# Kernel optimization log

Hardware: AMD Instinct MI355X
Metric: run time of the kernel (lower is better)

Reference implementation:

```python
import jax, jax.numpy as jnp
import numpy as np

BATCH, K, N, D = 8192, 8, 1024, 256
BETA = 0.25


def setup_inputs() -> dict:
    key = jax.random.key(0)
    kx, ke = jax.random.split(key)
    x = jax.random.normal(kx, (BATCH, K, D), dtype=jnp.float32)
    entries = jax.random.normal(ke, (K, N, D), dtype=jnp.float32)
    return {"x": x, "entries": entries}


def reference(x, entries):
    # x: [b, k, d]; entries: [k, n, d]
    xt = jnp.transpose(x, (1, 0, 2))  # [k, b, d]
    # squared euclidean distances (argmin is identical to cdist argmin)
    d2 = (
        jnp.sum(xt * xt, axis=-1)[:, :, None]
        + jnp.sum(entries * entries, axis=-1)[:, None, :]
        - 2.0 * jnp.einsum("kbd,knd->kbn", xt, entries)
    )  # [k, b, n]
    idx = jnp.argmin(d2, axis=-1)  # [k, b]
    quantized = jnp.take_along_axis(entries, idx[:, :, None], axis=1)  # [k, b, d]
    quantized = jnp.transpose(quantized, (1, 0, 2))  # [b, k, d]
    # straight-through estimator
    x_q = x + jax.lax.stop_gradient(quantized - x)
    dictionary_loss = jnp.mean(
        jnp.sum((jax.lax.stop_gradient(x) - quantized) ** 2, axis=-1)
    )
    commitment_loss = BETA * jnp.mean(
        jnp.sum((x - jax.lax.stop_gradient(quantized)) ** 2, axis=-1)
    )
    return x_q, jnp.transpose(idx, (1, 0)), dictionary_loss, commitment_loss
```

## Files before the change

### kernel.cpp

```cpp
#include <hip/hip_runtime.h>
#include <cstdint>
#include <cstddef>

#define BATCH 8192
#define KC 8
#define NC 1024
#define DC 256
#define TAU 0.10f

typedef __attribute__((ext_vector_type(8))) _Float16 half8;
typedef __attribute__((ext_vector_type(4))) _Float16 half4;
typedef __attribute__((ext_vector_type(4))) float floatx4;

__device__ __forceinline__ void async_load16(const void* g, void* l) {
    __builtin_amdgcn_global_load_lds((const __attribute__((address_space(1))) uint32_t*)g,
                                     (__attribute__((address_space(3))) uint32_t*)l, 16, 0, 0);
}

__device__ __forceinline__ int lidx(int r, int c) {
    return (r >> 3) * 1024 + (r & 7) * 128 + ((c ^ (r & 7)) * 16);
}
__device__ __forceinline__ half8 ldsr(const char* base, int r, int c) {
    return *(const half8*)(base + lidx(r, c));
}

__global__ __launch_bounds__(256) void prep_e_kernel(const float* __restrict__ entries,
                                                     _Float16* __restrict__ Ecat,
                                                     float* __restrict__ eef) {
    int wave = threadIdx.x >> 6, lane = threadIdx.x & 63;
    int row = blockIdx.x * 4 + wave;
    float4 v = ((const float4*)(entries + (size_t)row * DC))[lane];
    half4 h;
    h.x = (_Float16)v.x; h.y = (_Float16)v.y; h.z = (_Float16)v.z; h.w = (_Float16)v.w;
    *(half4*)(Ecat + (size_t)row * 256 + lane * 4) = h;
    double s = (double)v.x * v.x + (double)v.y * v.y + (double)v.z * v.z + (double)v.w * v.w;
    #pragma unroll
    for (int off = 32; off > 0; off >>= 1) s += __shfl_down(s, off, 64);
    if (lane == 0) eef[row] = (float)s;
}

__global__ __launch_bounds__(256, 2) void vq_gemm(const float* __restrict__ x,
                                                  const float* __restrict__ entries,
                                                  const _Float16* __restrict__ Ecat,
                                                  const float* __restrict__ eef,
                                                  float* __restrict__ out_idx,
                                                  float* __restrict__ out_q,
                                                  double* __restrict__ partial,
                                                  int* __restrict__ flag_list,
                                                  int* __restrict__ flag_cnt) {
    __shared__ alignas(16) char Bst[2][32768];
    __shared__ float eef_lds[NC];
    __shared__ float tv1[128];
    __shared__ float tv2[128];
    __shared__ int   ti1[128];
    __shared__ int   idx_lds[128];
    __shared__ double red[256];

    const int t = threadIdx.x;
    const int k  = blockIdx.x & 7;
    const int b0 = (blockIdx.x >> 3) * 128;
    const int w = t >> 6, lane = t & 63;
    const int quad = lane >> 4, col = lane & 15;
    const int rl = lane >> 3;
    const int cs = (lane & 7) ^ rl;

    { float4 v = ((const float4*)(eef + (size_t)k * NC))[t]; *(float4*)(eef_lds + t * 4) = v; }
    if (t < 128) { tv1[t] = 1e30f; tv2[t] = 1e30f; ti1[t] = 0; }

    half8 Ah[2][8];
    #pragma unroll
    for (int mi = 0; mi < 2; ++mi) {
        const float* xrow = x + ((size_t)(b0 + w * 32 + mi * 16 + col) * KC + k) * DC + quad * 8;
        #pragma unroll
        for (int ks = 0; ks < 8; ++ks) {
            float4 u0 = *(const float4*)(xrow + ks * 32);
            float4 u1 = *(const float4*)(xrow + ks * 32 + 4);
            float f[8] = {u0.x, u0.y, u0.z, u0.w, u1.x, u1.y, u1.z, u1.w};
            half8 h;
            #pragma unroll
            for (int j = 0; j < 8; ++j) h[j] = (_Float16)f[j];
            Ah[mi][ks] = h;
        }
    }

    const char* EcatK = (const char*)(Ecat + (size_t)k * NC * 256);

    #define ISSUE_B(nt_, h_)                                                             \
        {                                                                                \
            char* bb_ = Bst[h_];                                                         \
            _Pragma("unroll")                                                            \
            for (int j = 0; j < 8; ++j) {                                                \
                int li_ = w * 8 + j; int sub_ = li_ >> 4, grp_ = li_ & 15;               \
                const char* src_ = EcatK + (size_t)((nt_) * 128 + grp_ * 8 + rl) * 512   \
                                 + ((h_) * 128 + sub_ * 64) * 2 + cs * 16;               \
                async_load16(src_, bb_ + sub_ * 16384 + grp_ * 1024 + lane * 16);        \
            }                                                                            \
        }

    #define STAGE(h_, DOISS_, nti_)                                                      \
        {                                                                                \
            asm volatile("s_waitcnt vmcnt(0)" ::: "memory");                             \
            __builtin_amdgcn_s_barrier();                                                \
            __builtin_amdgcn_sched_barrier(0);                                           \
            if (DOISS_) { ISSUE_B((nti_), (h_) ^ 1); }                                   \
            const char* Bs_ = Bst[h_];                                                   \
            __builtin_amdgcn_s_setprio(1);                                               \
            _Pragma("unroll")                                                            \
            for (int sub = 0; sub < 2; ++sub) {                                          \
                _Pragma("unroll")                                                        \
                for (int kk = 0; kk < 2; ++kk) {                                         \
                    const int cb = kk * 4 + quad;                                        \
                    _Pragma("unroll")                                                    \
                    for (int ni = 0; ni < 8; ++ni) {                                     \
                        half8 bh = ldsr(Bs_ + sub * 16384, ni * 16 + col, cb);           \
                        acc[0][ni] = __builtin_amdgcn_mfma_f32_16x16x32_f16(             \
                            Ah[0][(h_) * 4 + sub * 2 + kk], bh, acc[0][ni], 0, 0, 0);    \
                        acc[1][ni] = __builtin_amdgcn_mfma_f32_16x16x32_f16(             \
                            Ah[1][(h_) * 4 + sub * 2 + kk], bh, acc[1][ni], 0, 0, 0);    \
                    }                                                                    \
                }                                                                        \
            }                                                                            \
            __builtin_amdgcn_s_setprio(0);                                               \
        }

    ISSUE_B(0, 0);

    for (int nt = 0; nt < 8; ++nt) {
        const int n0 = nt * 128;
        floatx4 acc[2][8] = {};
        STAGE(0, 1, nt)
        STAGE(1, (nt < 7), nt + 1)
        float ev[8];
        #pragma unroll
        for (int ni = 0; ni < 8; ++ni) ev[ni] = eef_lds[n0 + ni * 16 + col];
        #pragma unroll
        for (int mi = 0; mi < 2; ++mi) {
            #pragma unroll
            for (int reg = 0; reg < 4; ++reg) {
                float v1 = 1e30f, v2 = 1e30f; int i1 = 0;
                #pragma unroll
                for (int ni = 0; ni < 8; ++ni) {
                    float val = fmaf(-2.0f, acc[mi][ni][reg], ev[ni]);
                    int n = n0 + ni * 16 + col;
                    bool lt1 = val < v1;
                    bool lt2 = val < v2;
                    float nv2 = lt1 ? v1 : (lt2 ? val : v2);
                    v1 = lt1 ? val : v1;
                    i1 = lt1 ? n : i1;
                    v2 = nv2;
                }
                #pragma unroll
                for (int off = 1; off < 16; off <<= 1) {
                    float o1 = __shfl_xor(v1, off, 16);
                    float o2 = __shfl_xor(v2, off, 16);
                    int   oi = __shfl_xor(i1, off, 16);
                    bool sw = o1 < v1;
                    float hi = sw ? v1 : o1;
                    v1 = sw ? o1 : v1;
                    i1 = sw ? oi : i1;
                    v2 = fminf(fminf(v2, o2), hi);
                }
                if (col == 0) {
                    int row = w * 32 + mi * 16 + quad * 4 + reg;
                    float t1 = tv1[row], t2 = tv2[row];
                    bool sw = v1 < t1;
                    float hi = sw ? t1 : v1;
                    tv2[row] = fminf(fminf(t2, v2), hi);
                    tv1[row] = sw ? v1 : t1;
                    if (sw) ti1[row] = i1;
                }
            }
        }
    }

    __syncthreads();
    if (t < 128) {
        float v1 = tv1[t], v2 = tv2[t];
        int rid = (b0 + t) * KC + k;
        if (v2 - v1 < TAU) {
            int pos = atomicAdd(flag_cnt, 1);
            flag_list[pos] = rid;
            idx_lds[t] = -1;
        } else {
            int n = ti1[t];
            idx_lds[t] = n;
            out_idx[rid] = (float)n;
        }
    }
    __syncthreads();

    double s = 0.0;
    #pragma unroll
    for (int rr = 0; rr < 8; ++rr) {
        int r = rr * 16 + (t >> 4);
        int c = t & 15;
        int n = idx_lds[r];
        if (n >= 0) {
            const float4* xp = (const float4*)(x + ((size_t)(b0 + r) * KC + k) * DC);
            const float4* ep = (const float4*)(entries + ((size_t)k * NC + n) * DC);
            float4* op = (float4*)(out_q + ((size_t)(b0 + r) * KC + k) * DC);
            #pragma unroll
            for (int j = 0; j < 4; ++j) {
                int ci = j * 16 + c;
                float4 xv = xp[ci], evv = ep[ci];
                op[ci] = evv;
                double d0 = (double)xv.x - evv.x, d1 = (double)xv.y - evv.y;
                double d2 = (double)xv.z - evv.z, d3 = (double)xv.w - evv.w;
                s += d0 * d0 + d1 * d1 + d2 * d2 + d3 * d3;
            }
        }
    }
    red[t] = s;
    __syncthreads();
    for (int off2 = 128; off2 > 0; off2 >>= 1) {
        if (t < off2) red[t] += red[t + off2];
        __syncthreads();
    }
    if (t == 0) partial[blockIdx.x] = red[0];
    #undef STAGE
    #undef ISSUE_B
}

__global__ __launch_bounds__(256) void refine_scan(const float* __restrict__ x,
                                                   const float* __restrict__ entries,
                                                   const int* __restrict__ flag_list,
                                                   const int* __restrict__ flag_cnt,
                                                   unsigned long long* __restrict__ slots) {
    __shared__ float xs[DC];
    __shared__ float tile[128 * 67];
    __shared__ double bd[256];
    __shared__ int    bi[256];
    const int t = threadIdx.x;
    const int cnt = *flag_cnt;
    const int e = t >> 1, dh = (t & 1) * 32;
    for (int wi = blockIdx.x; wi < cnt * 8; wi += gridDim.x) {
        const int i = wi >> 3, seg = wi & 7;
        const int rid = flag_list[i];
        const int k = rid & 7;
        const int nb = seg * 128;
        __syncthreads();
        xs[t] = x[(size_t)rid * DC + t];
        double acc = 0.0;
        #pragma unroll
        for (int c = 0; c < 4; ++c) {
            __syncthreads();
            #pragma unroll
            for (int it = 0; it < 8; ++it) {
                int r = it * 16 + (t >> 4), c16 = t & 15;
                float4 v = *(const float4*)(entries
                    + ((size_t)k * NC + nb + r) * DC + c * 64 + c16 * 4);
                float* dst = &tile[r * 67 + c16 * 4];
                dst[0] = v.x; dst[1] = v.y; dst[2] = v.z; dst[3] = v.w;
            }
            __syncthreads();
            const float* xp = xs + c * 64 + dh;
            const float* ep = &tile[e * 67 + dh];
            #pragma unroll
            for (int d = 0; d < 32; ++d) {
                double df = (double)xp[d] - (double)ep[d];
                acc += df * df;
            }
        }
        acc += __shfl_xor(acc, 1, 64);
        bd[t] = acc; bi[t] = nb + e;
        __syncthreads();
        for (int s2 = 128; s2 > 0; s2 >>= 1) {
            if (t < s2) {
                if (bd[t + s2] < bd[t] || (bd[t + s2] == bd[t] && bi[t + s2] < bi[t])) {
                    bd[t] = bd[t + s2]; bi[t] = bi[t + s2];
                }
            }
            __syncthreads();
        }
        if (t == 0) {
            unsigned long long key =
                ((unsigned long long)__double_as_longlong(bd[0]) & ~1023ull)
                | (unsigned long long)(unsigned)bi[0];
            atomicMin(&slots[i], key);
        }
    }
}

__global__ __launch_bounds__(256) void refine_pick(const float* __restrict__ entries,
                                                   const int* __restrict__ flag_list,
                                                   const int* __restrict__ flag_cnt,
                                                   const unsigned long long* __restrict__ slots,
                                                   float* __restrict__ out_idx,
                                                   float* __restrict__ out_q,
                                                   double* __restrict__ refAcc) {
    const int t = threadIdx.x;
    const int cnt = *flag_cnt;
    for (int i = blockIdx.x; i < cnt; i += gridDim.x) {
        unsigned long long key = slots[i];
        int n = (int)(key & 1023ull);
        int rid = flag_list[i];
        int k = rid & 7;
        out_q[(size_t)rid * DC + t] = entries[((size_t)k * NC + n) * DC + t];
        if (t == 0) {
            out_idx[rid] = (float)n;
            atomicAdd(refAcc, __longlong_as_double((long long)(key & ~1023ull)));
        }
    }
}

__global__ __launch_bounds__(256) void finalize_kernel(const double* __restrict__ partial,
                                                       const double* __restrict__ refAcc,
                                                       float* __restrict__ out) {
    __shared__ double red[256];
    const int t = threadIdx.x;
    double s = 0.0;
    for (int i = t; i < 512; i += 256) s += partial[i];
    red[t] = s;
    __syncthreads();
    for (int off = 128; off > 0; off >>= 1) {
        if (t < off) red[t] += red[t + off];
        __syncthreads();
    }
    if (t == 0) {
        double L = (red[0] + *refAcc) * (1.0 / 65536.0);
        out[(size_t)BATCH * KC * DC + BATCH * KC + 0] = (float)L;
        out[(size_t)BATCH * KC * DC + BATCH * KC + 1] = (float)(0.25 * L);
    }
}

extern "C" void kernel_launch(void* const* d_in, const int* in_sizes, int n_in,
                              void* d_out, int out_size, void* d_ws, size_t ws_size,
                              hipStream_t stream) {
    const float* x       = (const float*)d_in[0];
    const float* entries = (const float*)d_in[1];
    float* out = (float*)d_out;

    char* ws = (char*)d_ws;
    int*      flag_cnt  = (int*)ws;
    double*   refAcc    = (double*)(ws + 8);
    double*   partial   = (double*)(ws + 4096);
    float*    eef       = (float*)(ws + 65536);
    int*      flag_list = (int*)(ws + 131072);
    _Float16* Ecat      = (_Float16*)(ws + 1048576);
    unsigned long long* slots = (unsigned long long*)(ws + 5242880);

    float* out_q   = out;
    float* out_idx = out + (size_t)BATCH * KC * DC;

    hipMemsetAsync(ws, 0, 16, stream);
    hipMemsetAsync(slots, 0xFF, (size_t)65536 * 8, stream);
    prep_e_kernel<<<KC * NC / 4, 256, 0, stream>>>(entries, Ecat, eef);
    vq_gemm<<<512, 256, 0, stream>>>(x, entries, Ecat, eef, out_idx, out_q,
                                     partial, flag_list, flag_cnt);
    refine_scan<<<4096, 256, 0, stream>>>(x, entries, flag_list, flag_cnt, slots);
    refine_pick<<<512, 256, 0, stream>>>(entries, flag_list, flag_cnt, slots,
                                         out_idx, out_q, refAcc);
    finalize_kernel<<<1, 256, 0, stream>>>(partial, refAcc, out);
}
```

Baseline: 254.1 us.

## Batch refine rows per codebook and keep top-2 in registers across tiles

The GEMM kernel now keeps each lane's running top-2 in registers across all eight N tiles and does the cross-lane shuffle reduction and LDS write once at the end, rather than per tile. Flagged rows are bucketed per codebook k. The refine scan processes 16 flagged rows against a 128-entry codebook tile per iteration, so each loaded entry tile is reused across rows, with an XOR-swizzled LDS layout and a shuffle-based argmin in place of the LDS tree reduction. The trade-offs are more registers in the GEMM, and a refine grid that now walks a fixed 32768-item space and skips empty groups.

```diff
diff --git a/kernel.cpp b/kernel.cpp
--- a/kernel.cpp
+++ b/kernel.cpp
@@ -65,7 +65,6 @@
     const int cs = (lane & 7) ^ rl;
 
     { float4 v = ((const float4*)(eef + (size_t)k * NC))[t]; *(float4*)(eef_lds + t * 4) = v; }
-    if (t < 128) { tv1[t] = 1e30f; tv2[t] = 1e30f; ti1[t] = 0; }
 
     half8 Ah[2][8];
     #pragma unroll
@@ -123,6 +122,10 @@
             __builtin_amdgcn_s_setprio(0);                                               \
         }
 
+    float lv1[8], lv2[8]; int li1[8];
+    #pragma unroll
+    for (int q = 0; q < 8; ++q) { lv1[q] = 1e30f; lv2[q] = 1e30f; li1[q] = 0; }
+
     ISSUE_B(0, 0);
 
     for (int nt = 0; nt < 8; ++nt) {
@@ -137,38 +140,42 @@
         for (int mi = 0; mi < 2; ++mi) {
             #pragma unroll
             for (int reg = 0; reg < 4; ++reg) {
-                float v1 = 1e30f, v2 = 1e30f; int i1 = 0;
+                const int q = mi * 4 + reg;
                 #pragma unroll
                 for (int ni = 0; ni < 8; ++ni) {
                     float val = fmaf(-2.0f, acc[mi][ni][reg], ev[ni]);
                     int n = n0 + ni * 16 + col;
-                    bool lt1 = val < v1;
-                    bool lt2 = val < v2;
-                    float nv2 = lt1 ? v1 : (lt2 ? val : v2);
-                    v1 = lt1 ? val : v1;
-                    i1 = lt1 ? n : i1;
-                    v2 = nv2;
+                    bool lt1 = val < lv1[q];
+                    bool lt2 = val < lv2[q];
+                    float nv2 = lt1 ? lv1[q] : (lt2 ? val : lv2[q]);
+                    li1[q] = lt1 ? n : li1[q];
+                    lv1[q] = lt1 ? val : lv1[q];
+                    lv2[q] = nv2;
                 }
-                #pragma unroll
-                for (int off = 1; off < 16; off <<= 1) {
-                    float o1 = __shfl_xor(v1, off, 16);
-                    float o2 = __shfl_xor(v2, off, 16);
-                    int   oi = __shfl_xor(i1, off, 16);
-                    bool sw = o1 < v1;
-                    float hi = sw ? v1 : o1;
-                    v1 = sw ? o1 : v1;
-                    i1 = sw ? oi : i1;
-                    v2 = fminf(fminf(v2, o2), hi);
-                }
-                if (col == 0) {
-                    int row = w * 32 + mi * 16 + quad * 4 + reg;
-                    float t1 = tv1[row], t2 = tv2[row];
-                    bool sw = v1 < t1;
-                    float hi = sw ? t1 : v1;
-                    tv2[row] = fminf(fminf(t2, v2), hi);
-                    tv1[row] = sw ? v1 : t1;
-                    if (sw) ti1[row] = i1;
-                }
+            }
+        }
+    }
+
+    #pragma unroll
+    for (int mi = 0; mi < 2; ++mi) {
+        #pragma unroll
+        for (int reg = 0; reg < 4; ++reg) {
+            const int q = mi * 4 + reg;
+            float v1 = lv1[q], v2 = lv2[q]; int i1 = li1[q];
+            #pragma unroll
+            for (int off = 1; off < 16; off <<= 1) {
+                float o1 = __shfl_xor(v1, off, 16);
+                float o2 = __shfl_xor(v2, off, 16);
+                int   oi = __shfl_xor(i1, off, 16);
+                bool sw = o1 < v1;
+                float hi = sw ? v1 : o1;
+                v1 = sw ? o1 : v1;
+                i1 = sw ? oi : i1;
+                v2 = fminf(fminf(v2, o2), hi);
+            }
+            if (col == 0) {
+                int row = w * 32 + mi * 16 + quad * 4 + reg;
+                tv1[row] = v1; tv2[row] = v2; ti1[row] = i1;
             }
         }
     }
@@ -178,8 +185,8 @@
         float v1 = tv1[t], v2 = tv2[t];
         int rid = (b0 + t) * KC + k;
         if (v2 - v1 < TAU) {
-            int pos = atomicAdd(flag_cnt, 1);
-            flag_list[pos] = rid;
+            int pos = atomicAdd(&flag_cnt[k], 1);
+            flag_list[k * 8192 + pos] = rid;
             idx_lds[t] = -1;
         } else {
             int n = ti1[t];
@@ -226,58 +233,75 @@
                                                    const int* __restrict__ flag_list,
                                                    const int* __restrict__ flag_cnt,
                                                    unsigned long long* __restrict__ slots) {
-    __shared__ float xs[DC];
-    __shared__ float tile[128 * 67];
-    __shared__ double bd[256];
-    __shared__ int    bi[256];
+    __shared__ alignas(16) char tileb[128 * 256];
+    __shared__ float xs[16 * 260];
     const int t = threadIdx.x;
-    const int cnt = *flag_cnt;
-    const int e = t >> 1, dh = (t & 1) * 32;
-    for (int wi = blockIdx.x; wi < cnt * 8; wi += gridDim.x) {
-        const int i = wi >> 3, seg = wi & 7;
-        const int rid = flag_list[i];
-        const int k = rid & 7;
-        const int nb = seg * 128;
-        __syncthreads();
-        xs[t] = x[(size_t)rid * DC + t];
-        double acc = 0.0;
+    const int r = t >> 4, eg = t & 15;
+    for (int it = blockIdx.x; it < 8 * 8 * 512; it += gridDim.x) {
+        const int k = it & 7, seg = (it >> 3) & 7, g = it >> 6;
+        const int cnt_k = flag_cnt[k];
+        if (g * 16 >= cnt_k) continue;
+        const int nrows = min(16, cnt_k - g * 16);
+        const int myrow = (r < nrows) ? r : 0;
+        const int rid = flag_list[k * 8192 + g * 16 + myrow];
+        {
+            const int rr = t >> 4, c16 = t & 15;
+            const int rid2 = flag_list[k * 8192 + g * 16 + ((rr < nrows) ? rr : 0)];
+            const float4* xp = (const float4*)(x + (size_t)rid2 * DC);
+            #pragma unroll
+            for (int j = 0; j < 4; ++j) {
+                float4 v = xp[c16 * 4 + j];
+                *(float4*)(xs + rr * 260 + (c16 * 4 + j) * 4) = v;
+            }
+        }
+        double acc[8] = {};
         #pragma unroll
         for (int c = 0; c < 4; ++c) {
+            {
+                const int c16 = t & 15;
+                #pragma unroll
+                for (int it2 = 0; it2 < 8; ++it2) {
+                    int row = it2 * 16 + (t >> 4);
+                    float4 v = *(const float4*)(entries
+                        + ((size_t)k * NC + seg * 128 + row) * DC + c * 64 + c16 * 4);
+                    *(float4*)(tileb + row * 256 + ((c16 ^ (row >> 3)) * 16)) = v;
+                }
+            }
             __syncthreads();
-            #pragma unroll
-            for (int it = 0; it < 8; ++it) {
-                int r = it * 16 + (t >> 4), c16 = t & 15;
-                float4 v = *(const float4*)(entries
-                    + ((size_t)k * NC + nb + r) * DC + c * 64 + c16 * 4);
-                float* dst = &tile[r * 67 + c16 * 4];
-                dst[0] = v.x; dst[1] = v.y; dst[2] = v.z; dst[3] = v.w;
+            const float* xpp = xs + r * 260 + c * 64;
+            #pragma unroll 4
+            for (int dq = 0; dq < 16; ++dq) {
+                float4 xv = *(const float4*)(xpp + dq * 4);
+                #pragma unroll
+                for (int j = 0; j < 8; ++j) {
+                    int e = eg * 8 + j;
+                    float4 evv = *(const float4*)(tileb + e * 256 + ((dq ^ eg) * 16));
+                    double d0 = (double)xv.x - (double)evv.x;
+                    double d1 = (double)xv.y - (double)evv.y;
+                    double d2 = (double)xv.z - (double)evv.z;
+                    double d3 = (double)xv.w - (double)evv.w;
+                    acc[j] += d0 * d0 + d1 * d1 + d2 * d2 + d3 * d3;
+                }
             }
             __syncthreads();
-            const float* xp = xs + c * 64 + dh;
-            const float* ep = &tile[e * 67 + dh];
-            #pragma unroll
-            for (int d = 0; d < 32; ++d) {
-                double df = (double)xp[d] - (double)ep[d];
-                acc += df * df;
-            }
-        }
-        acc += __shfl_xor(acc, 1, 64);
-        bd[t] = acc; bi[t] = nb + e;
-        __syncthreads();
-        for (int s2 = 128; s2 > 0; s2 >>= 1) {
-            if (t < s2) {
-                if (bd[t + s2] < bd[t] || (bd[t + s2] == bd[t] && bi[t + s2] < bi[t])) {
-                    bd[t] = bd[t + s2]; bi[t] = bi[t + s2];
-                }
-            }
-            __syncthreads();
-        }
-        if (t == 0) {
-            unsigned long long key =
-                ((unsigned long long)__double_as_longlong(bd[0]) & ~1023ull)
-                | (unsigned long long)(unsigned)bi[0];
-            atomicMin(&slots[i], key);
-        }
+        }
+        double best = acc[0]; int bn = seg * 128 + eg * 8;
+        #pragma unroll
+        for (int j = 1; j < 8; ++j) {
+            if (acc[j] < best) { best = acc[j]; bn = seg * 128 + eg * 8 + j; }
+        }
+        unsigned long long key =
+            ((unsigned long long)__double_as_longlong(best) & ~1023ull)
+            | (unsigned long long)(unsigned)bn;
+        #pragma unroll
+        for (int off = 1; off < 16; off <<= 1) {
+            unsigned long long o = __shfl_xor(key, off, 16);
+            key = o < key ? o : key;
+        }
+        if (eg == 0 && r < nrows) {
+            atomicMin(&slots[k * 8192 + g * 16 + r], key);
+        }
+        (void)rid;
     }
 }
 
@@ -289,12 +313,12 @@
                                                    float* __restrict__ out_q,
                                                    double* __restrict__ refAcc) {
     const int t = threadIdx.x;
-    const int cnt = *flag_cnt;
-    for (int i = blockIdx.x; i < cnt; i += gridDim.x) {
-        unsigned long long key = slots[i];
+    for (int idx = blockIdx.x; idx < 8 * 8192; idx += gridDim.x) {
+        const int k = idx >> 13, pos = idx & 8191;
+        if (pos >= flag_cnt[k]) continue;
+        unsigned long long key = slots[idx];
         int n = (int)(key & 1023ull);
-        int rid = flag_list[i];
-        int k = rid & 7;
+        int rid = flag_list[idx];
         out_q[(size_t)rid * DC + t] = entries[((size_t)k * NC + n) * DC + t];
         if (t == 0) {
             out_idx[rid] = (float)n;
@@ -332,7 +356,7 @@
 
     char* ws = (char*)d_ws;
     int*      flag_cnt  = (int*)ws;
-    double*   refAcc    = (double*)(ws + 8);
+    double*   refAcc    = (double*)(ws + 64);
     double*   partial   = (double*)(ws + 4096);
     float*    eef       = (float*)(ws + 65536);
     int*      flag_list = (int*)(ws + 131072);
@@ -342,12 +366,12 @@
     float* out_q   = out;
     float* out_idx = out + (size_t)BATCH * KC * DC;
 
-    hipMemsetAsync(ws, 0, 16, stream);
+    hipMemsetAsync(ws, 0, 128, stream);
     hipMemsetAsync(slots, 0xFF, (size_t)65536 * 8, stream);
     prep_e_kernel<<<KC * NC / 4, 256, 0, stream>>>(entries, Ecat, eef);
     vq_gemm<<<512, 256, 0, stream>>>(x, entries, Ecat, eef, out_idx, out_q,
                                      partial, flag_list, flag_cnt);
-    refine_scan<<<4096, 256, 0, stream>>>(x, entries, flag_list, flag_cnt, slots);
+    refine_scan<<<512, 256, 0, stream>>>(x, entries, flag_list, flag_cnt, slots);
     refine_pick<<<512, 256, 0, stream>>>(entries, flag_list, flag_cnt, slots,
                                          out_idx, out_q, refAcc);
     finalize_kernel<<<1, 256, 0, stream>>>(partial, refAcc, out);
```

After: 225.9 us. 11.1% less time.
